# Kernel tuning notes

Measured on AMD Instinct MI355X. Metric: run time of the kernel, lower is better.

The kernel has to match this reference:

```python
import jax, jax.numpy as jnp
import numpy as np

N_HEADS = 8
D_EMBED = 512
D_CROSS = 768
D_HEAD = D_EMBED // N_HEADS


def setup_inputs() -> dict:
    key = jax.random.key(0)
    ks = jax.random.split(key, 12)
    B, SQ, SKV = 8, 4096, 77
    s_e = 1.0 / np.sqrt(D_EMBED)
    s_c = 1.0 / np.sqrt(D_CROSS)
    return {
        "latent": jax.random.normal(ks[0], (B, SQ, D_EMBED), jnp.float32),
        "context": jax.random.normal(ks[1], (B, SKV, D_CROSS), jnp.float32),
        "wq": jax.random.normal(ks[2], (D_EMBED, D_EMBED), jnp.float32) * s_e,
        "bq": jax.random.normal(ks[3], (D_EMBED,), jnp.float32) * 0.01,
        "wk": jax.random.normal(ks[4], (D_CROSS, D_EMBED), jnp.float32) * s_c,
        "bk": jax.random.normal(ks[5], (D_EMBED,), jnp.float32) * 0.01,
        "wv": jax.random.normal(ks[6], (D_CROSS, D_EMBED), jnp.float32) * s_c,
        "bv": jax.random.normal(ks[7], (D_EMBED,), jnp.float32) * 0.01,
        "wo": jax.random.normal(ks[8], (D_EMBED, D_EMBED), jnp.float32) * s_e,
        "bo": jax.random.normal(ks[9], (D_EMBED,), jnp.float32) * 0.01,
    }


def reference(latent, context, wq, bq, wk, bk, wv, bv, wo, bo):
    B, SQ, _ = latent.shape
    SKV = context.shape[1]
    # projections; weights stored as (in, out)
    q = latent @ wq + bq                     # [B, SQ, D_EMBED]
    k = context @ wk + bk                    # [B, SKV, D_EMBED]
    v = context @ wv + bv                    # [B, SKV, D_EMBED]
    # split heads -> [B, H, S, Dh]
    q = q.reshape(B, SQ, N_HEADS, D_HEAD).transpose(0, 2, 1, 3)
    k = k.reshape(B, SKV, N_HEADS, D_HEAD).transpose(0, 2, 1, 3)
    v = v.reshape(B, SKV, N_HEADS, D_HEAD).transpose(0, 2, 1, 3)
    scale = 1.0 / np.sqrt(D_HEAD).astype(np.float32)
    w = jnp.einsum("bhqd,bhkd->bhqk", q, k) * scale  # [B, H, SQ, SKV]
    w = jax.nn.softmax(w, axis=-1)
    out = jnp.einsum("bhqk,bhkd->bhqd", w, v)        # [B, H, SQ, Dh]
    out = out.transpose(0, 2, 1, 3).reshape(B, SQ, D_EMBED)
    return out @ wo + bo
```

## Files before the change

### kernel.cpp

```cpp
#include <hip/hip_runtime.h>


typedef __attribute__((ext_vector_type(8))) __bf16 bf16x8;
typedef __attribute__((ext_vector_type(4))) float f32x4;

#define DEVI static __device__ __forceinline__

typedef __attribute__((address_space(3))) void lds_void_t;
typedef const __attribute__((address_space(1))) void gbl_void_t;
#define GLDS16(gsrc, ldst) \
  __builtin_amdgcn_global_load_lds((gbl_void_t*)(gsrc), (lds_void_t*)(ldst), 16, 0, 0)

DEVI unsigned short f2bf(float f) {
  unsigned int u = __float_as_uint(f);
  u += 0x7FFFu + ((u >> 16) & 1u);
  return (unsigned short)(u >> 16);
}

DEVI unsigned int pack2bf(float a, float b) {
  return (unsigned int)f2bf(a) | ((unsigned int)f2bf(b) << 16);
}

__global__ __launch_bounds__(256) void wtrans_all_kernel(
    const float* __restrict__ wq, const float* __restrict__ wk,
    const float* __restrict__ wv, const float* __restrict__ wo,
    unsigned short* __restrict__ wqT, unsigned short* __restrict__ wkT,
    unsigned short* __restrict__ wvT, unsigned short* __restrict__ woT) {
  __shared__ float tile[32][33];
  int bid = blockIdx.x;
  const float* in;
  unsigned short* out;
  int K, r;
  if (bid < 256)       { in = wq; out = wqT; K = 512; r = bid; }
  else if (bid < 640)  { in = wk; out = wkT; K = 768; r = bid - 256; }
  else if (bid < 1024) { in = wv; out = wvT; K = 768; r = bid - 640; }
  else                 { in = wo; out = woT; K = 512; r = bid - 1024; }
  int n0 = (r & 15) * 32, k0 = (r >> 4) * 32;
  int tx = threadIdx.x, ty = threadIdx.y;
#pragma unroll
  for (int j = 0; j < 4; ++j)
    tile[ty * 4 + j][tx] = in[(size_t)(k0 + ty * 4 + j) * 512 + n0 + tx];
  __syncthreads();
#pragma unroll
  for (int j = 0; j < 4; ++j)
    out[(size_t)(n0 + ty * 4 + j) * K + k0 + tx] = f2bf(tile[tx][ty * 4 + j]);
}

__global__ __launch_bounds__(256) void kv_proj_kernel(const float* __restrict__ ctx,
                                                      const unsigned short* __restrict__ wkT,
                                                      const unsigned short* __restrict__ wvT,
                                                      const float* __restrict__ bk,
                                                      const float* __restrict__ bv,
                                                      unsigned short* __restrict__ Kp,
                                                      unsigned short* __restrict__ Vt) {
  __shared__ __align__(16) unsigned short As[64][40];
  __shared__ __align__(16) unsigned short Bs[64][40];
  int bid = blockIdx.x;
  int sel = bid / 80;
  int rem = bid % 80;
  int mt = rem / 8, nt = rem % 8;
  const unsigned short* wT = sel ? wvT : wkT;
  const float* bias = sel ? bv : bk;
  int tid = threadIdx.x;
  int l = tid & 63, w = tid >> 6;
  int lr = l & 15, lg = l >> 4;

  f32x4 acc[4] = {};
  for (int k0 = 0; k0 < 768; k0 += 32) {
#pragma unroll
    for (int it = 0; it < 2; ++it) {
      int idx4 = it * 256 + tid;
      int r = idx4 >> 3, q4 = idx4 & 7;
      int m = mt * 64 + r;
      float4 v = {0.f, 0.f, 0.f, 0.f};
      if (m < 616) v = *(const float4*)(ctx + (size_t)m * 768 + k0 + q4 * 4);
      ushort4 o;
      o.x = f2bf(v.x); o.y = f2bf(v.y); o.z = f2bf(v.z); o.w = f2bf(v.w);
      *(ushort4*)&As[r][q4 * 4] = o;
    }
    {
      int c = tid >> 2, q8 = tid & 3;
      *(uint4*)&Bs[c][q8 * 8] =
          *(const uint4*)(wT + (size_t)(nt * 64 + c) * 768 + k0 + q8 * 8);
    }
    __syncthreads();
    bf16x8 a = *(const bf16x8*)&As[w * 16 + lr][lg * 8];
#pragma unroll
    for (int n = 0; n < 4; ++n) {
      bf16x8 bb = *(const bf16x8*)&Bs[n * 16 + lr][lg * 8];
      acc[n] = __builtin_amdgcn_mfma_f32_16x16x32_bf16(a, bb, acc[n], 0, 0, 0);
    }
    __syncthreads();
  }
#pragma unroll
  for (int n = 0; n < 4; ++n) {
#pragma unroll
    for (int reg = 0; reg < 4; ++reg) {
      int m = mt * 64 + w * 16 + lg * 4 + reg;
      if (m < 616) {
        int bI = m / 77, s = m % 77;
        int col = nt * 64 + n * 16 + lr;
        int h = col >> 6, d = col & 63;
        float v = acc[n][reg] + bias[col];
        if (sel == 0)
          Kp[(((size_t)(bI * 8 + h)) * 80 + s) * 64 + d] = f2bf(v);
        else
          Vt[(((size_t)(bI * 8 + h)) * 64 + d) * 96 + s] = f2bf(v);
      }
    }
  }
}

__global__ __launch_bounds__(256, 4) void qproj_attn_kernel(
    const float* __restrict__ A32, const unsigned short* __restrict__ BT,
    const float* __restrict__ bias, const unsigned short* __restrict__ Kp,
    const unsigned short* __restrict__ Vt, unsigned short* __restrict__ Oq) {
  __shared__ __align__(16) char smem[36864];
  unsigned short* As = (unsigned short*)smem;
  unsigned short* Bs = (unsigned short*)(smem + 16384);
  unsigned short* Qw = (unsigned short*)smem;

  int bid = ((blockIdx.x & 7) << 7) | (blockIdx.x >> 3);
  size_t mbase = (size_t)(bid >> 2) * 128;
  int nbase = (bid & 3) * 128;
  int tid = threadIdx.x;
  int l = tid & 63, w = tid >> 6;
  int lr = l & 15, lg = l >> 4;
  int wr = (w >> 1) * 64, wc = (w & 1) * 64;

  const float* pA0 = A32 + (mbase + (tid >> 2)) * 512 + (tid & 3) * 8;
  const float* pA1 = pA0 + (size_t)64 * 512;
  const unsigned short* gB = BT + (size_t)(nbase + w * 32 + (l >> 2)) * 512 + (l & 3) * 8;

  {
    float4 x0 = *(const float4*)(pA0);
    float4 x1 = *(const float4*)(pA0 + 4);
    float4 x2 = *(const float4*)(pA1);
    float4 x3 = *(const float4*)(pA1 + 4);
    GLDS16(gB, Bs + w * 1024);
    GLDS16(gB + 16 * 512, Bs + w * 1024 + 512);
    uint4 u0, u1;
    u0.x = pack2bf(x0.x, x0.y); u0.y = pack2bf(x0.z, x0.w);
    u0.z = pack2bf(x1.x, x1.y); u0.w = pack2bf(x1.z, x1.w);
    u1.x = pack2bf(x2.x, x2.y); u1.y = pack2bf(x2.z, x2.w);
    u1.z = pack2bf(x3.x, x3.y); u1.w = pack2bf(x3.z, x3.w);
    *(uint4*)&As[tid * 8] = u0;
    *(uint4*)&As[tid * 8 + 2048] = u1;
  }
  __syncthreads();

  f32x4 acc[4][4] = {};
#pragma unroll
  for (int k0 = 0; k0 < 512; k0 += 32) {
    const int cur = (k0 >> 5) & 1;
    const int nxt = cur ^ 1;
    unsigned short* curA = As + cur * 4096;
    unsigned short* curB = Bs + cur * 4096;
    const bool more = (k0 < 480);
    float4 x0, x1, x2, x3;
    if (more) {
      x0 = *(const float4*)(pA0 + k0 + 32);
      x1 = *(const float4*)(pA0 + k0 + 36);
      x2 = *(const float4*)(pA1 + k0 + 32);
      x3 = *(const float4*)(pA1 + k0 + 36);
      GLDS16(gB + k0 + 32, Bs + nxt * 4096 + w * 1024);
      GLDS16(gB + k0 + 32 + 16 * 512, Bs + nxt * 4096 + w * 1024 + 512);
    }
    bf16x8 af[4], bv8[4];
#pragma unroll
    for (int m = 0; m < 4; ++m)
      af[m] = *(const bf16x8*)&curA[(wr + m * 16 + lr) * 32 + lg * 8];
#pragma unroll
    for (int n = 0; n < 4; ++n)
      bv8[n] = *(const bf16x8*)&curB[(wc + n * 16 + lr) * 32 + lg * 8];
#pragma unroll
    for (int m = 0; m < 4; ++m)
#pragma unroll
      for (int n = 0; n < 4; ++n)
        acc[m][n] = __builtin_amdgcn_mfma_f32_16x16x32_bf16(af[m], bv8[n], acc[m][n], 0, 0, 0);
    if (more) {
      uint4 u0, u1;
      u0.x = pack2bf(x0.x, x0.y); u0.y = pack2bf(x0.z, x0.w);
      u0.z = pack2bf(x1.x, x1.y); u0.w = pack2bf(x1.z, x1.w);
      u1.x = pack2bf(x2.x, x2.y); u1.y = pack2bf(x2.z, x2.w);
      u1.z = pack2bf(x3.x, x3.y); u1.w = pack2bf(x3.z, x3.w);
      *(uint4*)&As[nxt * 4096 + tid * 8] = u0;
      *(uint4*)&As[nxt * 4096 + tid * 8 + 2048] = u1;
    }
    __syncthreads();
  }

  unsigned short* Qme = Qw + w * (64 * 72);
  float bb[4];
#pragma unroll
  for (int n = 0; n < 4; ++n) bb[n] = bias[nbase + wc + n * 16 + lr];
#pragma unroll
  for (int m = 0; m < 4; ++m)
#pragma unroll
    for (int n = 0; n < 4; ++n)
#pragma unroll
      for (int reg = 0; reg < 4; ++reg)
        Qme[(m * 16 + lg * 4 + reg) * 72 + n * 16 + lr] = f2bf(acc[m][n][reg] + bb[n]);

  bf16x8 qf[4][2];
#pragma unroll
  for (int rg = 0; rg < 4; ++rg) {
    qf[rg][0] = *(const bf16x8*)&Qme[(rg * 16 + lr) * 72 + lg * 8];
    qf[rg][1] = *(const bf16x8*)&Qme[(rg * 16 + lr) * 72 + 32 + lg * 8];
  }
  __syncthreads();

  unsigned short* Pme = (unsigned short*)smem + w * 1664;
  for (int z = l; z < 256; z += 64) Pme[(z >> 4) * 104 + 80 + (z & 15)] = 0;

  int b = (int)(mbase >> 12);
  int h = (bid & 3) * 2 + (w & 1);
  const unsigned short* Kph = Kp + (size_t)(b * 8 + h) * (80 * 64);
  const unsigned short* Vth = Vt + (size_t)(b * 8 + h) * (64 * 96);

  const float C = 0.125f * 1.44269504088896f;

  auto QK = [&](int rg, f32x4* s) {
#pragma unroll
    for (int t = 0; t < 5; ++t) {
      const unsigned short* kr = Kph + (t * 16 + lr) * 64 + lg * 8;
      bf16x8 k0 = *(const bf16x8*)kr;
      bf16x8 k1 = *(const bf16x8*)(kr + 32);
      s[t] = __builtin_amdgcn_mfma_f32_16x16x32_bf16(qf[rg][0], k0, s[t], 0, 0, 0);
      s[t] = __builtin_amdgcn_mfma_f32_16x16x32_bf16(qf[rg][1], k1, s[t], 0, 0, 0);
    }
    if (lr >= 13) {
      s[4][0] = -1e30f; s[4][1] = -1e30f; s[4][2] = -1e30f; s[4][3] = -1e30f;
    }
  };

  f32x4 sc[5] = {};
  QK(0, sc);
#pragma unroll
  for (int rg = 0; rg < 4; ++rg) {
    float mx[4], sm[4];
#pragma unroll
    for (int r = 0; r < 4; ++r)
      mx[r] = fmaxf(fmaxf(fmaxf(sc[0][r], sc[1][r]), fmaxf(sc[2][r], sc[3][r])), sc[4][r]);
#pragma unroll
    for (int d = 1; d < 16; d <<= 1)
#pragma unroll
      for (int r = 0; r < 4; ++r) mx[r] = fmaxf(mx[r], __shfl_xor(mx[r], d, 64));
    float p[5][4];
#pragma unroll
    for (int t = 0; t < 5; ++t)
#pragma unroll
      for (int r = 0; r < 4; ++r) p[t][r] = exp2f((sc[t][r] - mx[r]) * C);
#pragma unroll
    for (int r = 0; r < 4; ++r)
      sm[r] = p[0][r] + p[1][r] + p[2][r] + p[3][r] + p[4][r];
#pragma unroll
    for (int d = 1; d < 16; d <<= 1)
#pragma unroll
      for (int r = 0; r < 4; ++r) sm[r] += __shfl_xor(sm[r], d, 64);
#pragma unroll
    for (int r = 0; r < 4; ++r) sm[r] = 1.0f / sm[r];
#pragma unroll
    for (int t = 0; t < 5; ++t)
#pragma unroll
      for (int r = 0; r < 4; ++r)
        Pme[(lg * 4 + r) * 104 + t * 16 + lr] = f2bf(p[t][r] * sm[r]);

    f32x4 sn[5] = {};
    if (rg < 3) QK(rg + 1, sn);

    bf16x8 ap[3];
#pragma unroll
    for (int c = 0; c < 3; ++c) ap[c] = *(const bf16x8*)&Pme[lr * 104 + c * 32 + lg * 8];
#pragma unroll
    for (int ct = 0; ct < 4; ++ct) {
      f32x4 o = {};
#pragma unroll
      for (int c = 0; c < 3; ++c) {
        bf16x8 vv = *(const bf16x8*)(Vth + (size_t)(ct * 16 + lr) * 96 + c * 32 + lg * 8);
        o = __builtin_amdgcn_mfma_f32_16x16x32_bf16(ap[c], vv, o, 0, 0, 0);
      }
#pragma unroll
      for (int reg = 0; reg < 4; ++reg)
        Oq[(mbase + wr + rg * 16 + lg * 4 + reg) * 512 + nbase + wc + ct * 16 + lr] =
            f2bf(o[reg]);
    }
#pragma unroll
    for (int t = 0; t < 5; ++t) sc[t] = sn[t];
  }
}

__global__ __launch_bounds__(256) void gemm512_glds_kernel(
    const unsigned short* __restrict__ A, const unsigned short* __restrict__ BT,
    const float* __restrict__ bias, float* __restrict__ Out) {
  __shared__ __align__(16) unsigned short As[128 * 32];
  __shared__ __align__(16) unsigned short Bs[128 * 32];
  int bid = ((blockIdx.x & 7) << 7) | (blockIdx.x >> 3);
  size_t mbase = (size_t)(bid >> 2) * 128;
  int nbase = (bid & 3) * 128;
  int tid = threadIdx.x;
  int l = tid & 63, w = tid >> 6;
  int lr = l & 15, lg = l >> 4;
  int wr = (w >> 1) * 64, wc = (w & 1) * 64;

  const unsigned short* gA = A + (mbase + w * 32 + (l >> 2)) * 512 + (l & 3) * 8;
  const unsigned short* gB = BT + (size_t)(nbase + w * 32 + (l >> 2)) * 512 + (l & 3) * 8;
  unsigned short* lA = As + w * 1024;
  unsigned short* lB = Bs + w * 1024;

  f32x4 acc[4][4] = {};
  for (int k0 = 0; k0 < 512; k0 += 32) {
    GLDS16(gA + k0, lA);
    GLDS16(gA + k0 + 16 * 512, lA + 512);
    GLDS16(gB + k0, lB);
    GLDS16(gB + k0 + 16 * 512, lB + 512);
    asm volatile("s_waitcnt vmcnt(0)" ::: "memory");
    __syncthreads();
    bf16x8 af[4], bv8[4];
#pragma unroll
    for (int m = 0; m < 4; ++m)
      af[m] = *(const bf16x8*)&As[(wr + m * 16 + lr) * 32 + lg * 8];
#pragma unroll
    for (int n = 0; n < 4; ++n)
      bv8[n] = *(const bf16x8*)&Bs[(wc + n * 16 + lr) * 32 + lg * 8];
#pragma unroll
    for (int m = 0; m < 4; ++m)
#pragma unroll
      for (int n = 0; n < 4; ++n)
        acc[m][n] = __builtin_amdgcn_mfma_f32_16x16x32_bf16(af[m], bv8[n], acc[m][n], 0, 0, 0);
    __syncthreads();
  }
#pragma unroll
  for (int m = 0; m < 4; ++m) {
#pragma unroll
    for (int n = 0; n < 4; ++n) {
#pragma unroll
      for (int reg = 0; reg < 4; ++reg) {
        size_t row = mbase + wr + m * 16 + lg * 4 + reg;
        int col = nbase + wc + n * 16 + lr;
        Out[row * 512 + col] = acc[m][n][reg] + bias[col];
      }
    }
  }
}

static const size_t OFF_Q   = 0;
static const size_t OFF_KP  = 33554432;
static const size_t OFF_VT  = OFF_KP + 655360;
static const size_t OFF_WQT = OFF_VT + 786432;
static const size_t OFF_WKT = OFF_WQT + 524288;
static const size_t OFF_WVT = OFF_WKT + 786432;
static const size_t OFF_WOT = OFF_WVT + 786432;
static const size_t WS_NEEDED = OFF_WOT + 524288;

extern "C" void kernel_launch(void* const* d_in, const int* in_sizes, int n_in,
                              void* d_out, int out_size, void* d_ws, size_t ws_size,
                              hipStream_t stream) {
  (void)in_sizes; (void)n_in; (void)out_size;
  if (ws_size < WS_NEEDED) return;

  const float* latent  = (const float*)d_in[0];
  const float* context = (const float*)d_in[1];
  const float* wq = (const float*)d_in[2];
  const float* bq = (const float*)d_in[3];
  const float* wk = (const float*)d_in[4];
  const float* bk = (const float*)d_in[5];
  const float* wv = (const float*)d_in[6];
  const float* bv = (const float*)d_in[7];
  const float* wo = (const float*)d_in[8];
  const float* bo = (const float*)d_in[9];
  float* out = (float*)d_out;

  char* ws = (char*)d_ws;
  unsigned short* wsQ = (unsigned short*)(ws + OFF_Q);
  unsigned short* Kp  = (unsigned short*)(ws + OFF_KP);
  unsigned short* Vt  = (unsigned short*)(ws + OFF_VT);
  unsigned short* wqT = (unsigned short*)(ws + OFF_WQT);
  unsigned short* wkT = (unsigned short*)(ws + OFF_WKT);
  unsigned short* wvT = (unsigned short*)(ws + OFF_WVT);
  unsigned short* woT = (unsigned short*)(ws + OFF_WOT);

  wtrans_all_kernel<<<1280, dim3(32, 8), 0, stream>>>(wq, wk, wv, wo,
                                                      wqT, wkT, wvT, woT);
  hipMemsetAsync(ws + OFF_KP, 0, 655360 + 786432, stream);
  kv_proj_kernel<<<160, 256, 0, stream>>>(context, wkT, wvT, bk, bv, Kp, Vt);
  qproj_attn_kernel<<<1024, 256, 0, stream>>>(latent, wqT, bq, Kp, Vt, wsQ);
  gemm512_glds_kernel<<<1024, 256, 0, stream>>>(wsQ, woT, bo, out);
}
```

Baseline: 122.3 us.

## Pre-convert latent to bf16, use async LDS loads, double-buffer output GEMM, defer softmax normalization

Adds a separate kernel that converts the fp32 latent to bf16 and stores it in the output buffer as scratch. The Q-projection main loop can then stream A through global_load_lds instead of doing register loads and in-loop packing. The output GEMM gets double-buffered LDS with prefetch of the next K slice, and softmax normalization moves from the probabilities to the PV output. This trades an extra full pass over latent (read fp32, write bf16) for simpler, more overlapped GEMM loops and drops a barrier by reusing each wave's own LDS region for P.

```diff
diff --git a/kernel.cpp b/kernel.cpp
--- a/kernel.cpp
+++ b/kernel.cpp
@@ -19,6 +19,20 @@
 
 DEVI unsigned int pack2bf(float a, float b) {
   return (unsigned int)f2bf(a) | ((unsigned int)f2bf(b) << 16);
+}
+
+__global__ __launch_bounds__(256) void cvt_bf16_kernel(const float* __restrict__ in,
+                                                       unsigned int* __restrict__ out4) {
+  int i = blockIdx.x * 256 + threadIdx.x;
+  const float4* in4 = (const float4*)in;
+  float4 a = in4[2 * i];
+  float4 b = in4[2 * i + 1];
+  uint4 o;
+  o.x = pack2bf(a.x, a.y);
+  o.y = pack2bf(a.z, a.w);
+  o.z = pack2bf(b.x, b.y);
+  o.w = pack2bf(b.z, b.w);
+  *(uint4*)(out4 + 4 * (size_t)i) = o;
 }
 
 __global__ __launch_bounds__(256) void wtrans_all_kernel(
@@ -112,13 +126,12 @@
 }
 
 __global__ __launch_bounds__(256, 4) void qproj_attn_kernel(
-    const float* __restrict__ A32, const unsigned short* __restrict__ BT,
+    const unsigned short* __restrict__ A, const unsigned short* __restrict__ BT,
     const float* __restrict__ bias, const unsigned short* __restrict__ Kp,
     const unsigned short* __restrict__ Vt, unsigned short* __restrict__ Oq) {
   __shared__ __align__(16) char smem[36864];
   unsigned short* As = (unsigned short*)smem;
   unsigned short* Bs = (unsigned short*)(smem + 16384);
-  unsigned short* Qw = (unsigned short*)smem;
 
   int bid = ((blockIdx.x & 7) << 7) | (blockIdx.x >> 3);
   size_t mbase = (size_t)(bid >> 2) * 128;
@@ -128,25 +141,14 @@
   int lr = l & 15, lg = l >> 4;
   int wr = (w >> 1) * 64, wc = (w & 1) * 64;
 
-  const float* pA0 = A32 + (mbase + (tid >> 2)) * 512 + (tid & 3) * 8;
-  const float* pA1 = pA0 + (size_t)64 * 512;
+  const unsigned short* gA = A + (mbase + w * 32 + (l >> 2)) * 512 + (l & 3) * 8;
   const unsigned short* gB = BT + (size_t)(nbase + w * 32 + (l >> 2)) * 512 + (l & 3) * 8;
 
-  {
-    float4 x0 = *(const float4*)(pA0);
-    float4 x1 = *(const float4*)(pA0 + 4);
-    float4 x2 = *(const float4*)(pA1);
-    float4 x3 = *(const float4*)(pA1 + 4);
-    GLDS16(gB, Bs + w * 1024);
-    GLDS16(gB + 16 * 512, Bs + w * 1024 + 512);
-    uint4 u0, u1;
-    u0.x = pack2bf(x0.x, x0.y); u0.y = pack2bf(x0.z, x0.w);
-    u0.z = pack2bf(x1.x, x1.y); u0.w = pack2bf(x1.z, x1.w);
-    u1.x = pack2bf(x2.x, x2.y); u1.y = pack2bf(x2.z, x2.w);
-    u1.z = pack2bf(x3.x, x3.y); u1.w = pack2bf(x3.z, x3.w);
-    *(uint4*)&As[tid * 8] = u0;
-    *(uint4*)&As[tid * 8 + 2048] = u1;
-  }
+  GLDS16(gA, As + w * 1024);
+  GLDS16(gA + 16 * 512, As + w * 1024 + 512);
+  GLDS16(gB, Bs + w * 1024);
+  GLDS16(gB + 16 * 512, Bs + w * 1024 + 512);
+  asm volatile("s_waitcnt vmcnt(0)" ::: "memory");
   __syncthreads();
 
   f32x4 acc[4][4] = {};
@@ -154,18 +156,14 @@
   for (int k0 = 0; k0 < 512; k0 += 32) {
     const int cur = (k0 >> 5) & 1;
     const int nxt = cur ^ 1;
-    unsigned short* curA = As + cur * 4096;
-    unsigned short* curB = Bs + cur * 4096;
-    const bool more = (k0 < 480);
-    float4 x0, x1, x2, x3;
-    if (more) {
-      x0 = *(const float4*)(pA0 + k0 + 32);
-      x1 = *(const float4*)(pA0 + k0 + 36);
-      x2 = *(const float4*)(pA1 + k0 + 32);
-      x3 = *(const float4*)(pA1 + k0 + 36);
+    if (k0 < 480) {
+      GLDS16(gA + k0 + 32, As + nxt * 4096 + w * 1024);
+      GLDS16(gA + k0 + 32 + 16 * 512, As + nxt * 4096 + w * 1024 + 512);
       GLDS16(gB + k0 + 32, Bs + nxt * 4096 + w * 1024);
       GLDS16(gB + k0 + 32 + 16 * 512, Bs + nxt * 4096 + w * 1024 + 512);
     }
+    const unsigned short* curA = As + cur * 4096;
+    const unsigned short* curB = Bs + cur * 4096;
     bf16x8 af[4], bv8[4];
 #pragma unroll
     for (int m = 0; m < 4; ++m)
@@ -178,19 +176,11 @@
 #pragma unroll
       for (int n = 0; n < 4; ++n)
         acc[m][n] = __builtin_amdgcn_mfma_f32_16x16x32_bf16(af[m], bv8[n], acc[m][n], 0, 0, 0);
-    if (more) {
-      uint4 u0, u1;
-      u0.x = pack2bf(x0.x, x0.y); u0.y = pack2bf(x0.z, x0.w);
-      u0.z = pack2bf(x1.x, x1.y); u0.w = pack2bf(x1.z, x1.w);
-      u1.x = pack2bf(x2.x, x2.y); u1.y = pack2bf(x2.z, x2.w);
-      u1.z = pack2bf(x3.x, x3.y); u1.w = pack2bf(x3.z, x3.w);
-      *(uint4*)&As[nxt * 4096 + tid * 8] = u0;
-      *(uint4*)&As[nxt * 4096 + tid * 8 + 2048] = u1;
-    }
+    asm volatile("s_waitcnt vmcnt(0)" ::: "memory");
     __syncthreads();
   }
 
-  unsigned short* Qme = Qw + w * (64 * 72);
+  unsigned short* Qme = (unsigned short*)smem + w * (64 * 72);
   float bb[4];
 #pragma unroll
   for (int n = 0; n < 4; ++n) bb[n] = bias[nbase + wc + n * 16 + lr];
@@ -208,9 +198,8 @@
     qf[rg][0] = *(const bf16x8*)&Qme[(rg * 16 + lr) * 72 + lg * 8];
     qf[rg][1] = *(const bf16x8*)&Qme[(rg * 16 + lr) * 72 + 32 + lg * 8];
   }
-  __syncthreads();
-
-  unsigned short* Pme = (unsigned short*)smem + w * 1664;
+
+  unsigned short* Pme = Qme;
   for (int z = l; z < 256; z += 64) Pme[(z >> 4) * 104 + 80 + (z & 15)] = 0;
 
   int b = (int)(mbase >> 12);
@@ -238,7 +227,7 @@
   QK(0, sc);
 #pragma unroll
   for (int rg = 0; rg < 4; ++rg) {
-    float mx[4], sm[4];
+    float mx[4];
 #pragma unroll
     for (int r = 0; r < 4; ++r)
       mx[r] = fmaxf(fmaxf(fmaxf(sc[0][r], sc[1][r]), fmaxf(sc[2][r], sc[3][r])), sc[4][r]);
@@ -252,19 +241,22 @@
 #pragma unroll
       for (int r = 0; r < 4; ++r) p[t][r] = exp2f((sc[t][r] - mx[r]) * C);
 #pragma unroll
+    for (int t = 0; t < 5; ++t)
+#pragma unroll
+      for (int r = 0; r < 4; ++r)
+        Pme[(lg * 4 + r) * 104 + t * 16 + lr] = f2bf(p[t][r]);
+
+    float sm[4];
+#pragma unroll
     for (int r = 0; r < 4; ++r)
       sm[r] = p[0][r] + p[1][r] + p[2][r] + p[3][r] + p[4][r];
 #pragma unroll
     for (int d = 1; d < 16; d <<= 1)
 #pragma unroll
       for (int r = 0; r < 4; ++r) sm[r] += __shfl_xor(sm[r], d, 64);
-#pragma unroll
-    for (int r = 0; r < 4; ++r) sm[r] = 1.0f / sm[r];
-#pragma unroll
-    for (int t = 0; t < 5; ++t)
-#pragma unroll
-      for (int r = 0; r < 4; ++r)
-        Pme[(lg * 4 + r) * 104 + t * 16 + lr] = f2bf(p[t][r] * sm[r]);
+    float rs[4];
+#pragma unroll
+    for (int r = 0; r < 4; ++r) rs[r] = 1.0f / sm[r];
 
     f32x4 sn[5] = {};
     if (rg < 3) QK(rg + 1, sn);
@@ -283,7 +275,7 @@
 #pragma unroll
       for (int reg = 0; reg < 4; ++reg)
         Oq[(mbase + wr + rg * 16 + lg * 4 + reg) * 512 + nbase + wc + ct * 16 + lr] =
-            f2bf(o[reg]);
+            f2bf(o[reg] * rs[reg]);
     }
 #pragma unroll
     for (int t = 0; t < 5; ++t) sc[t] = sn[t];
@@ -293,8 +285,8 @@
 __global__ __launch_bounds__(256) void gemm512_glds_kernel(
     const unsigned short* __restrict__ A, const unsigned short* __restrict__ BT,
     const float* __restrict__ bias, float* __restrict__ Out) {
-  __shared__ __align__(16) unsigned short As[128 * 32];
-  __shared__ __align__(16) unsigned short Bs[128 * 32];
+  __shared__ __align__(16) unsigned short As[2][128 * 32];
+  __shared__ __align__(16) unsigned short Bs[2][128 * 32];
   int bid = ((blockIdx.x & 7) << 7) | (blockIdx.x >> 3);
   size_t mbase = (size_t)(bid >> 2) * 128;
   int nbase = (bid & 3) * 128;
@@ -305,29 +297,38 @@
 
   const unsigned short* gA = A + (mbase + w * 32 + (l >> 2)) * 512 + (l & 3) * 8;
   const unsigned short* gB = BT + (size_t)(nbase + w * 32 + (l >> 2)) * 512 + (l & 3) * 8;
-  unsigned short* lA = As + w * 1024;
-  unsigned short* lB = Bs + w * 1024;
+
+  GLDS16(gA, As[0] + w * 1024);
+  GLDS16(gA + 16 * 512, As[0] + w * 1024 + 512);
+  GLDS16(gB, Bs[0] + w * 1024);
+  GLDS16(gB + 16 * 512, Bs[0] + w * 1024 + 512);
+  asm volatile("s_waitcnt vmcnt(0)" ::: "memory");
+  __syncthreads();
 
   f32x4 acc[4][4] = {};
+#pragma unroll
   for (int k0 = 0; k0 < 512; k0 += 32) {
-    GLDS16(gA + k0, lA);
-    GLDS16(gA + k0 + 16 * 512, lA + 512);
-    GLDS16(gB + k0, lB);
-    GLDS16(gB + k0 + 16 * 512, lB + 512);
-    asm volatile("s_waitcnt vmcnt(0)" ::: "memory");
-    __syncthreads();
+    const int cur = (k0 >> 5) & 1;
+    const int nxt = cur ^ 1;
+    if (k0 < 480) {
+      GLDS16(gA + k0 + 32, As[nxt] + w * 1024);
+      GLDS16(gA + k0 + 32 + 16 * 512, As[nxt] + w * 1024 + 512);
+      GLDS16(gB + k0 + 32, Bs[nxt] + w * 1024);
+      GLDS16(gB + k0 + 32 + 16 * 512, Bs[nxt] + w * 1024 + 512);
+    }
     bf16x8 af[4], bv8[4];
 #pragma unroll
     for (int m = 0; m < 4; ++m)
-      af[m] = *(const bf16x8*)&As[(wr + m * 16 + lr) * 32 + lg * 8];
+      af[m] = *(const bf16x8*)&As[cur][(wr + m * 16 + lr) * 32 + lg * 8];
 #pragma unroll
     for (int n = 0; n < 4; ++n)
-      bv8[n] = *(const bf16x8*)&Bs[(wc + n * 16 + lr) * 32 + lg * 8];
+      bv8[n] = *(const bf16x8*)&Bs[cur][(wc + n * 16 + lr) * 32 + lg * 8];
 #pragma unroll
     for (int m = 0; m < 4; ++m)
 #pragma unroll
       for (int n = 0; n < 4; ++n)
         acc[m][n] = __builtin_amdgcn_mfma_f32_16x16x32_bf16(af[m], bv8[n], acc[m][n], 0, 0, 0);
+    asm volatile("s_waitcnt vmcnt(0)" ::: "memory");
     __syncthreads();
   }
 #pragma unroll
@@ -380,10 +381,13 @@
   unsigned short* wvT = (unsigned short*)(ws + OFF_WVT);
   unsigned short* woT = (unsigned short*)(ws + OFF_WOT);
 
+  unsigned short* latBF = (unsigned short*)d_out;
+
   wtrans_all_kernel<<<1280, dim3(32, 8), 0, stream>>>(wq, wk, wv, wo,
                                                       wqT, wkT, wvT, woT);
   hipMemsetAsync(ws + OFF_KP, 0, 655360 + 786432, stream);
   kv_proj_kernel<<<160, 256, 0, stream>>>(context, wkT, wvT, bk, bv, Kp, Vt);
-  qproj_attn_kernel<<<1024, 256, 0, stream>>>(latent, wqT, bq, Kp, Vt, wsQ);
+  cvt_bf16_kernel<<<8192, 256, 0, stream>>>(latent, (unsigned int*)latBF);
+  qproj_attn_kernel<<<1024, 256, 0, stream>>>(latBF, wqT, bq, Kp, Vt, wsQ);
   gemm512_glds_kernel<<<1024, 256, 0, stream>>>(wsQ, woT, bo, out);
 }
```

Result: slower. 127.1 us (+3.9%).
